# Kernel tuning notes

Hardware: AMD Instinct MI355X
Metric: run time of the kernel (lower is better)

## Reference

```python
import jax, jax.numpy as jnp
import numpy as np

S, D, H = 1024, 512, 4
DK = D // H  # 128
POOL = 16
EPS = 1e-5


def _pos_encoding(seq_len, dmodel):
    pos = jnp.arange(seq_len, dtype=jnp.float32)[:, None]
    div = jnp.exp(jnp.arange(0, dmodel, 2, dtype=jnp.float32) * (-jnp.log(10000.0) / dmodel))
    ang = pos * div  # [S, D/2]
    # interleave sin/cos -> pe[:,0::2]=sin, pe[:,1::2]=cos
    return jnp.stack([jnp.sin(ang), jnp.cos(ang)], axis=-1).reshape(seq_len, dmodel)


def _layernorm(x, g, b):
    mu = jnp.mean(x, axis=-1, keepdims=True)
    var = jnp.var(x, axis=-1, keepdims=True)
    return (x - mu) * jax.lax.rsqrt(var + EPS) * g + b


def setup_inputs() -> dict:
    key = jax.random.key(0)
    ks = jax.random.split(key, 16)
    u = lambda k, shape, r: jax.random.uniform(k, shape, jnp.float32, -r, r)
    nfeature = 512
    return {
        "x": jax.random.normal(ks[0], (16, S, nfeature), jnp.float32),
        "emb_w": u(ks[1], (nfeature, D), (1.0 / nfeature) ** 0.5),
        "emb_b": u(ks[2], (D,), (1.0 / nfeature) ** 0.5),
        "WQ": u(ks[3], (H, D, DK), 0.1),
        "WK": u(ks[4], (H, D, DK), 0.1),
        "WV": u(ks[5], (H, D, DK), 0.1),
        "WO": u(ks[6], (H * DK, D), 0.1),
        "g1": jnp.ones((D,), jnp.float32),
        "b1": jnp.zeros((D,), jnp.float32),
        "l1_w": u(ks[7], (D, 4 * D), (1.0 / D) ** 0.5),
        "l1_b": u(ks[8], (4 * D,), (1.0 / D) ** 0.5),
        "l2_w": u(ks[9], (4 * D, D), (1.0 / (4 * D)) ** 0.5),
        "l2_b": u(ks[10], (D,), (1.0 / (4 * D)) ** 0.5),
        "g2": jnp.ones((D,), jnp.float32),
        "b2": jnp.zeros((D,), jnp.float32),
        "fc_w": u(ks[11], (S * (D // POOL), 2), 0.1),
        "fc_b": jnp.zeros((2,), jnp.float32),
    }


def reference(x, emb_w, emb_b, WQ, WK, WV, WO, g1, b1, l1_w, l1_b, l2_w, l2_b, g2, b2, fc_w, fc_b):
    # dropout layers are identity (eval mode)
    h = x @ emb_w + emb_b                       # [B,S,D]
    h = h.reshape(-1, S, D) + _pos_encoding(S, D)
    inp = h
    # per-head projections (hand-rolled MHA)
    Qi = jnp.einsum('bsd,hde->bhse', h, WQ)     # [B,H,S,DK]
    Ki = jnp.einsum('bsd,hde->bhse', h, WK)
    Vi = jnp.einsum('bsd,hde->bhse', h, WV)
    scores = jnp.einsum('bhse,bhte->bhst', Qi, Ki) / jnp.sqrt(jnp.float32(DK))
    attn = jax.nn.softmax(scores, axis=-1)      # [B,H,S,S] -- full attention matrix, as in source
    head = jnp.einsum('bhst,bhte->bhse', attn, Vi)  # [B,H,S,DK]
    # NOTE: source does a raw reshape [B,H,S,DK] -> [B,S,H*DK] (no transpose); replicate exactly
    out = head.reshape(-1, S, H * DK) @ WO      # [B,S,D]
    h = _layernorm(out + inp, g1, b1)
    ffn = jax.nn.relu(h @ l1_w + l1_b) @ l2_w + l2_b
    h = _layernorm(ffn + h, g2, b2)
    # MaxPool1d(16,16) over the feature dim: [B,S,512] -> [B,S,32]
    pooled = h.reshape(-1, S, D // POOL, POOL).max(axis=-1)
    logits = pooled.reshape(-1, S * (D // POOL)) @ fc_w + fc_b  # [B,2]
    return jax.nn.log_softmax(logits, axis=-1)
```

## Files before the change

### kernel.cpp

```cpp
#include <hip/hip_runtime.h>

typedef unsigned short ushortb;
typedef __attribute__((ext_vector_type(8))) short short8;
typedef __attribute__((ext_vector_type(4))) float f32x4;

__device__ __forceinline__ ushortb f2bb(float f) {
    union { float f; unsigned u; } x; x.f = f;
    unsigned r = x.u + 0x7fffu + ((x.u >> 16) & 1u);
    return (ushortb)(r >> 16);
}
__device__ __forceinline__ float bb2f(ushortb u) {
    union { unsigned u; float f; } x; x.u = ((unsigned)u) << 16; return x.f;
}

__device__ __forceinline__ unsigned pkbb(float a, float b) {
#if __has_builtin(__builtin_amdgcn_cvt_pk_bf16_f32)
    auto p = __builtin_amdgcn_cvt_pk_bf16_f32(a, b);
    unsigned u; __builtin_memcpy(&u, &p, 4);
    return u;
#else
    return (unsigned)f2bb(a) | ((unsigned)f2bb(b) << 16);
#endif
}

#if __has_builtin(__builtin_amdgcn_exp2f)
#define EXP2(x) __builtin_amdgcn_exp2f(x)
#else
#define EXP2(x) exp2f(x)
#endif

__device__ __forceinline__ void async_ld16(void* lds, const void* g) {
    __builtin_amdgcn_global_load_lds(
        (const __attribute__((address_space(1))) void*)g,
        (__attribute__((address_space(3))) void*)lds, 16, 0, 0);
}

#define EP_EMB       0
#define EP_RES       2
#define EP_BIAS_RELU 3
#define EP_BIAS_RES  4
#define EP_QKV       7

template <int EP>
__global__ __launch_bounds__(256) void gemm_mfma(
    const ushortb* __restrict__ A, const ushortb* __restrict__ Bt,
    const float* __restrict__ bias, const ushortb* __restrict__ res,
    const float* __restrict__ pe, ushortb* __restrict__ C,
    int M, int N, int K)
{
    __shared__ ushortb sA[2][128][64];
    __shared__ ushortb sB[2][128][64];

    const int tid = threadIdx.x;
    const int wave = tid >> 6, lane = tid & 63;
    const int quad = lane >> 4, l15 = lane & 15;
    const int row0 = blockIdx.x * 128;
    const int col0 = blockIdx.y * 128;
    const int wm = (wave >> 1) * 64, wn = (wave & 1) * 64;
    const int srl = lane >> 3, slot = lane & 7;

    f32x4 acc[4][4];
    #pragma unroll
    for (int i = 0; i < 4; ++i)
        #pragma unroll
        for (int j = 0; j < 4; ++j) acc[i][j] = (f32x4){0.f, 0.f, 0.f, 0.f};

    #pragma unroll
    for (int c = 0; c < 4; ++c) {
        int rbase = wave * 32 + c * 8;
        int r = rbase + srl;
        int ka = (slot ^ ((r ^ (r >> 3)) & 7)) * 8;
        async_ld16(&sA[0][rbase][0], A  + (size_t)(row0 + r) * K + ka);
        async_ld16(&sB[0][rbase][0], Bt + (size_t)(col0 + r) * K + ka);
    }

    int buf = 0;
    for (int k0 = 0; k0 < K; k0 += 64) {
        __syncthreads();
        if (k0 + 64 < K) {
            int nb = buf ^ 1;
            #pragma unroll
            for (int c = 0; c < 4; ++c) {
                int rbase = wave * 32 + c * 8;
                int r = rbase + srl;
                int ka = (slot ^ ((r ^ (r >> 3)) & 7)) * 8;
                async_ld16(&sA[nb][rbase][0], A  + (size_t)(row0 + r) * K + k0 + 64 + ka);
                async_ld16(&sB[nb][rbase][0], Bt + (size_t)(col0 + r) * K + k0 + 64 + ka);
            }
        }
        #pragma unroll
        for (int kc = 0; kc < 2; ++kc) {
            short8 af[4], bf[4];
            #pragma unroll
            for (int i = 0; i < 4; ++i) {
                int m = wm + i * 16 + l15;
                af[i] = *(const short8*)&sA[buf][m][(((kc * 4 + quad) ^ ((m ^ (m >> 3)) & 7))) * 8];
            }
            #pragma unroll
            for (int j = 0; j < 4; ++j) {
                int n = wn + j * 16 + l15;
                bf[j] = *(const short8*)&sB[buf][n][(((kc * 4 + quad) ^ ((n ^ (n >> 3)) & 7))) * 8];
            }
            #pragma unroll
            for (int i = 0; i < 4; ++i)
                #pragma unroll
                for (int j = 0; j < 4; ++j)
                    acc[i][j] = __builtin_amdgcn_mfma_f32_16x16x32_bf16(af[i], bf[j], acc[i][j], 0, 0, 0);
        }
        buf ^= 1;
    }

    if constexpr (EP == EP_QKV) {
        if (col0 < 1024) {
            ushortb* dst = C + ((size_t)(col0 >> 9)) * ((size_t)M * 512);
            #pragma unroll
            for (int i = 0; i < 4; ++i)
                #pragma unroll
                for (int r = 0; r < 4; ++r) {
                    int row = row0 + wm + i * 16 + quad * 4 + r;
                    #pragma unroll
                    for (int j = 0; j < 4; ++j) {
                        int col = (col0 + wn + j * 16 + l15) & 511;
                        dst[(size_t)row * 512 + col] = f2bb(acc[i][j][r]);
                    }
                }
        } else {
            ushortb* Vt = C + (size_t)2 * M * 512;
            int bb_ = row0 >> 10;
            #pragma unroll
            for (int i = 0; i < 4; ++i) {
                int s = (row0 & 1023) + wm + i * 16 + quad * 4;
                #pragma unroll
                for (int j = 0; j < 4; ++j) {
                    int vcol = col0 + wn + j * 16 + l15 - 1024;
                    int h = vcol >> 7, e = vcol & 127;
                    uint2 v;
                    v.x = pkbb(acc[i][j][0], acc[i][j][1]);
                    v.y = pkbb(acc[i][j][2], acc[i][j][3]);
                    *(uint2*)&Vt[((size_t)((bb_ * 4 + h) * 128 + e) << 10) + s] = v;
                }
            }
        }
        return;
    }

    #pragma unroll
    for (int i = 0; i < 4; ++i) {
        #pragma unroll
        for (int r = 0; r < 4; ++r) {
            int row = row0 + wm + i * 16 + quad * 4 + r;
            #pragma unroll
            for (int j = 0; j < 4; ++j) {
                int col = col0 + wn + j * 16 + l15;
                float v = acc[i][j][r];
                if constexpr (EP == EP_EMB) {
                    v += bias[col] + pe[((row & 1023) << 9) + col];
                } else if constexpr (EP == EP_RES) {
                    v += bb2f(res[(size_t)row * N + col]);
                } else if constexpr (EP == EP_BIAS_RELU) {
                    v = fmaxf(v + bias[col], 0.0f);
                } else if constexpr (EP == EP_BIAS_RES) {
                    v += bias[col] + bb2f(res[(size_t)row * N + col]);
                }
                C[(size_t)row * N + col] = f2bb(v);
            }
        }
    }
}

__global__ __launch_bounds__(256) void conv_x(const float* __restrict__ in,
                                              ushortb* __restrict__ out)
{
    size_t i4 = (size_t)blockIdx.x * 256 + threadIdx.x;
    float4 v = *(const float4*)(in + i4 * 4);
    ushort4 o;
    o.x = f2bb(v.x); o.y = f2bb(v.y); o.z = f2bb(v.z); o.w = f2bb(v.w);
    *(ushort4*)(out + i4 * 4) = o;
}

__global__ __launch_bounds__(256) void tileT(const float* __restrict__ in,
                                             ushortb* __restrict__ out,
                                             int R, int C, float scale)
{
    __shared__ float t[64][65];
    const int tx = threadIdx.x & 63, ty = threadIdx.x >> 6;
    const int c0 = blockIdx.x * 64, r0 = blockIdx.y * 64;
    const size_t zoff = (size_t)blockIdx.z * R * C;
    #pragma unroll
    for (int i = 0; i < 16; ++i) {
        int r = ty + i * 4;
        t[r][tx] = in[zoff + (size_t)(r0 + r) * C + c0 + tx] * scale;
    }
    __syncthreads();
    #pragma unroll
    for (int i = 0; i < 16; ++i) {
        int r = ty + i * 4;
        out[zoff + (size_t)(c0 + r) * R + r0 + tx] = f2bb(t[tx][r]);
    }
}

__global__ __launch_bounds__(256) void pairT512(const float* __restrict__ emb_w,
                                                const float* __restrict__ WO,
                                                ushortb* __restrict__ embwt,
                                                ushortb* __restrict__ wot)
{
    __shared__ float t[64][65];
    const int tx = threadIdx.x & 63, ty = threadIdx.x >> 6;
    const int c0 = blockIdx.x * 64, r0 = blockIdx.y * 64;
    const float* in = blockIdx.z ? WO : emb_w;
    ushortb* out = blockIdx.z ? wot : embwt;
    #pragma unroll
    for (int i = 0; i < 16; ++i) {
        int r = ty + i * 4;
        t[r][tx] = in[(size_t)(r0 + r) * 512 + c0 + tx];
    }
    __syncthreads();
    #pragma unroll
    for (int i = 0; i < 16; ++i) {
        int r = ty + i * 4;
        out[(size_t)(c0 + r) * 512 + r0 + tx] = f2bb(t[tx][r]);
    }
}

__global__ __launch_bounds__(256) void qkvT(const float* __restrict__ WQ,
                                            const float* __restrict__ WK,
                                            const float* __restrict__ WV,
                                            ushortb* __restrict__ wqkvt,
                                            float qscale)
{
    __shared__ float t[64][65];
    const int tx = threadIdx.x & 63, ty = threadIdx.x >> 6;
    const int c0 = blockIdx.x * 64, r0 = blockIdx.y * 64;
    const int z = blockIdx.z, sel = z >> 2, zz = z & 3;
    const float* in = (sel == 0 ? WQ : (sel == 1 ? WK : WV)) + (size_t)zz * 65536;
    ushortb* out = wqkvt + (size_t)sel * 262144 + (size_t)zz * 65536;
    const float scale = (sel == 0) ? qscale : 1.0f;
    #pragma unroll
    for (int i = 0; i < 16; ++i) {
        int r = ty + i * 4;
        t[r][tx] = in[(size_t)(r0 + r) * 128 + c0 + tx] * scale;
    }
    __syncthreads();
    #pragma unroll
    for (int i = 0; i < 16; ++i) {
        int r = ty + i * 4;
        out[(size_t)(c0 + r) * 512 + r0 + tx] = f2bb(t[tx][r]);
    }
}

__global__ __launch_bounds__(256) void pe_kernel(float* __restrict__ pe)
{
    int idx = blockIdx.x * 256 + threadIdx.x;
    int s = idx >> 9, c = idx & 511;
    float div = expf((float)(c & ~1) * (-9.210340371976184f / 512.0f));
    float ang = (float)s * div;
    pe[idx] = (c & 1) ? cosf(ang) : sinf(ang);
}

__global__ __launch_bounds__(256) void attn_mfma(
    const ushortb* __restrict__ Qb, const ushortb* __restrict__ Kb,
    const ushortb* __restrict__ Vt, ushortb* __restrict__ O)
{
    __shared__ ushortb sK[2][32][128];
    __shared__ ushortb sVt[2][128][32];
    __shared__ ushortb sP[4][32][40];

    const int tid = threadIdx.x;
    const int wave = tid >> 6, lane = tid & 63;
    const int quad = lane >> 4, l15 = lane & 15;
    const int bid = blockIdx.x;
    const int bh = bid & 63, qc = bid >> 6;
    const int b = bh >> 2, h = bh & 3;
    const int q0 = qc * 128 + wave * 32;
    const size_t qk_off = ((size_t)b << 10) * 512 + h * 128;
    const ushortb* Qp = Qb + qk_off;
    const ushortb* Kp = Kb + qk_off;
    const ushortb* Vp = Vt + (((size_t)(b * 4 + h)) << 17);

    short8 qfA[4], qfB[4];
    {
        const ushortb* qa = Qp + (size_t)(q0 + l15) * 512;
        const ushortb* qb = Qp + (size_t)(q0 + 16 + l15) * 512;
        #pragma unroll
        for (int kc = 0; kc < 4; ++kc) {
            qfA[kc] = *(const short8*)(qa + kc * 32 + quad * 8);
            qfB[kc] = *(const short8*)(qb + kc * 32 + quad * 8);
        }
    }

    f32x4 oA[8], oB[8];
    #pragma unroll
    for (int dt = 0; dt < 8; ++dt) {
        oA[dt] = (f32x4){0.f, 0.f, 0.f, 0.f};
        oB[dt] = (f32x4){0.f, 0.f, 0.f, 0.f};
    }
    float lA = 0.f, lB = 0.f;

    #pragma unroll
    for (int c = 0; c < 2; ++c) {
        int seg = wave * 2 + c;
        int rk = seg * 4 + (lane >> 4);
        int ck = (lane & 15) ^ (rk & 15);
        async_ld16(&sK[0][seg * 4][0], Kp + (size_t)rk * 512 + ck * 8);
        int dv = seg * 16 + (lane >> 2);
        int cv = (lane & 3) ^ (dv & 3);
        async_ld16(&sVt[0][seg * 16][0], Vp + ((size_t)dv << 10) + cv * 8);
    }

    int buf = 0;
    for (int t0 = 0; t0 < 1024; t0 += 32) {
        __syncthreads();
        if (t0 + 32 < 1024) {
            int nb = buf ^ 1;
            #pragma unroll
            for (int c = 0; c < 2; ++c) {
                int seg = wave * 2 + c;
                int rk = seg * 4 + (lane >> 4);
                int ck = (lane & 15) ^ (rk & 15);
                async_ld16(&sK[nb][seg * 4][0], Kp + (size_t)(t0 + 32 + rk) * 512 + ck * 8);
                int dv = seg * 16 + (lane >> 2);
                int cv = (lane & 3) ^ (dv & 3);
                async_ld16(&sVt[nb][seg * 16][0], Vp + ((size_t)dv << 10) + t0 + 32 + cv * 8);
            }
        }

        f32x4 sA0 = {0,0,0,0}, sA1 = {0,0,0,0}, sB0 = {0,0,0,0}, sB1 = {0,0,0,0};
        #pragma unroll
        for (int kc = 0; kc < 4; ++kc) {
            short8 k0f = *(const short8*)&sK[buf][l15][((kc * 4 + quad) ^ l15) * 8];
            short8 k1f = *(const short8*)&sK[buf][16 + l15][((kc * 4 + quad) ^ l15) * 8];
            sA0 = __builtin_amdgcn_mfma_f32_16x16x32_bf16(k0f, qfA[kc], sA0, 0, 0, 0);
            sA1 = __builtin_amdgcn_mfma_f32_16x16x32_bf16(k1f, qfA[kc], sA1, 0, 0, 0);
            sB0 = __builtin_amdgcn_mfma_f32_16x16x32_bf16(k0f, qfB[kc], sB0, 0, 0, 0);
            sB1 = __builtin_amdgcn_mfma_f32_16x16x32_bf16(k1f, qfB[kc], sB1, 0, 0, 0);
        }

        float pA0[4], pA1[4], pB0[4], pB1[4];
        float sumA = 0.f, sumB = 0.f;
        #pragma unroll
        for (int r = 0; r < 4; ++r) {
            pA0[r] = EXP2(sA0[r]); pA1[r] = EXP2(sA1[r]);
            pB0[r] = EXP2(sB0[r]); pB1[r] = EXP2(sB1[r]);
            sumA += pA0[r] + pA1[r];
            sumB += pB0[r] + pB1[r];
        }
        lA += sumA; lB += sumB;

        uint2 w;
        w.x = pkbb(pA0[0], pA0[1]); w.y = pkbb(pA0[2], pA0[3]);
        *(uint2*)&sP[wave][l15][quad * 4] = w;
        w.x = pkbb(pA1[0], pA1[1]); w.y = pkbb(pA1[2], pA1[3]);
        *(uint2*)&sP[wave][l15][16 + quad * 4] = w;
        w.x = pkbb(pB0[0], pB0[1]); w.y = pkbb(pB0[2], pB0[3]);
        *(uint2*)&sP[wave][16 + l15][quad * 4] = w;
        w.x = pkbb(pB1[0], pB1[1]); w.y = pkbb(pB1[2], pB1[3]);
        *(uint2*)&sP[wave][16 + l15][16 + quad * 4] = w;

        short8 pfA = *(const short8*)&sP[wave][l15][quad * 8];
        short8 pfB = *(const short8*)&sP[wave][16 + l15][quad * 8];

        #pragma unroll
        for (int dt = 0; dt < 8; ++dt) {
            int d = dt * 16 + l15;
            short8 vfrag = *(const short8*)&sVt[buf][d][(quad ^ (d & 3)) * 8];
            oA[dt] = __builtin_amdgcn_mfma_f32_16x16x32_bf16(pfA, vfrag, oA[dt], 0, 0, 0);
            oB[dt] = __builtin_amdgcn_mfma_f32_16x16x32_bf16(pfB, vfrag, oB[dt], 0, 0, 0);
        }
        buf ^= 1;
    }

    lA += __shfl_xor(lA, 16); lA += __shfl_xor(lA, 32);
    lB += __shfl_xor(lB, 16); lB += __shfl_xor(lB, 32);

    const size_t obase = (((size_t)(b * 4 + h) << 10) + q0) << 7;
    #pragma unroll
    for (int r = 0; r < 4; ++r) {
        float invA = 1.0f / __shfl(lA, quad * 4 + r);
        float invB = 1.0f / __shfl(lB, quad * 4 + r);
        int qa = quad * 4 + r, qb = 16 + quad * 4 + r;
        #pragma unroll
        for (int dt = 0; dt < 8; ++dt) {
            O[obase + ((size_t)qa << 7) + dt * 16 + l15] = f2bb(oA[dt][r] * invA);
            O[obase + ((size_t)qb << 7) + dt * 16 + l15] = f2bb(oB[dt][r] * invB);
        }
    }
}

__global__ __launch_bounds__(256) void ln_kernel(const ushortb* __restrict__ in,
                                                 const float* __restrict__ g,
                                                 const float* __restrict__ bta,
                                                 ushortb* __restrict__ out)
{
    const int lane = threadIdx.x & 63, w = threadIdx.x >> 6;
    const size_t row = (size_t)blockIdx.x * 4 + w;
    const int e0 = lane * 8;
    short8 v8 = *(const short8*)(in + row * 512 + e0);
    float v[8];
    #pragma unroll
    for (int k = 0; k < 8; ++k) v[k] = bb2f((ushortb)((short*)&v8)[k]);
    float s = 0.f, sq = 0.f;
    #pragma unroll
    for (int k = 0; k < 8; ++k) { s += v[k]; sq += v[k] * v[k]; }
    #pragma unroll
    for (int o = 1; o < 64; o <<= 1) { s += __shfl_xor(s, o); sq += __shfl_xor(sq, o); }
    float mu = s * (1.0f / 512.0f);
    float var = sq * (1.0f / 512.0f) - mu * mu;
    float rstd = rsqrtf(var + 1e-5f);
    float4 g0 = *(const float4*)(g + e0),  g1 = *(const float4*)(g + e0 + 4);
    float4 b0 = *(const float4*)(bta + e0), b1 = *(const float4*)(bta + e0 + 4);
    float gg[8] = {g0.x, g0.y, g0.z, g0.w, g1.x, g1.y, g1.z, g1.w};
    float bb[8] = {b0.x, b0.y, b0.z, b0.w, b1.x, b1.y, b1.z, b1.w};
    short8 o8;
    #pragma unroll
    for (int k = 0; k < 8; ++k)
        ((short*)&o8)[k] = (short)f2bb((v[k] - mu) * rstd * gg[k] + bb[k]);
    *(short8*)(out + row * 512 + e0) = o8;
}

__global__ __launch_bounds__(256) void final_partial(const ushortb* __restrict__ ln2,
                                                     const float* __restrict__ fcw,
                                                     float* __restrict__ zbuf)
{
    const int b = blockIdx.x, chunk = blockIdx.y;
    const int tid = threadIdx.x;
    float a0 = 0.0f, a1 = 0.0f;
    #pragma unroll
    for (int t = 0; t < 8; ++t) {
        int m = chunk * 2048 + t * 256 + tid;
        int s = m >> 5, j = m & 31;
        const ushortb* p = ln2 + (((size_t)(b * 1024 + s)) << 9) + j * 16;
        float mx = -1e30f;
        #pragma unroll
        for (int e = 0; e < 16; ++e) mx = fmaxf(mx, bb2f(p[e]));
        a0 += mx * fcw[2 * m];
        a1 += mx * fcw[2 * m + 1];
    }
    __shared__ float r0[256], r1[256];
    r0[tid] = a0; r1[tid] = a1;
    __syncthreads();
    for (int o = 128; o > 0; o >>= 1) {
        if (tid < o) { r0[tid] += r0[tid + o]; r1[tid] += r1[tid + o]; }
        __syncthreads();
    }
    if (tid == 0) {
        atomicAdd(&zbuf[2 * b],     r0[0]);
        atomicAdd(&zbuf[2 * b + 1], r1[0]);
    }
}

__global__ __launch_bounds__(64) void final_logits(const float* __restrict__ zbuf,
                                                   const float* __restrict__ fcb,
                                                   float* __restrict__ out)
{
    int b = threadIdx.x;
    if (b < 16) {
        float z0 = zbuf[2 * b]     + fcb[0];
        float z1 = zbuf[2 * b + 1] + fcb[1];
        float mx = fmaxf(z0, z1);
        float lse = mx + logf(expf(z0 - mx) + expf(z1 - mx));
        out[2 * b]     = z0 - lse;
        out[2 * b + 1] = z1 - lse;
    }
}

extern "C" void kernel_launch(void* const* d_in, const int* in_sizes, int n_in,
                              void* d_out, int out_size, void* d_ws, size_t ws_size,
                              hipStream_t stream)
{
    const float* x     = (const float*)d_in[0];
    const float* emb_w = (const float*)d_in[1];
    const float* emb_b = (const float*)d_in[2];
    const float* WQ    = (const float*)d_in[3];
    const float* WK    = (const float*)d_in[4];
    const float* WV    = (const float*)d_in[5];
    const float* WO    = (const float*)d_in[6];
    const float* g1    = (const float*)d_in[7];
    const float* b1    = (const float*)d_in[8];
    const float* l1w   = (const float*)d_in[9];
    const float* l1b   = (const float*)d_in[10];
    const float* l2w   = (const float*)d_in[11];
    const float* l2b   = (const float*)d_in[12];
    const float* g2    = (const float*)d_in[13];
    const float* b2    = (const float*)d_in[14];
    const float* fcw   = (const float*)d_in[15];
    const float* fcb   = (const float*)d_in[16];
    float* out = (float*)d_out;

    char* ws = (char*)d_ws;
    const size_t Ub = (size_t)16384 * 512 * 2;
    ushortb* xb    = (ushortb*)(ws + 0 * Ub);
    ushortb* h0b   = (ushortb*)(ws + 1 * Ub);
    ushortb* Qb    = (ushortb*)(ws + 2 * Ub);
    ushortb* Kb    = (ushortb*)(ws + 3 * Ub);
    ushortb* Vt    = (ushortb*)(ws + 4 * Ub);
    ushortb* headR = (ushortb*)(ws + 5 * Ub);
    ushortb* mid   = (ushortb*)(ws + 3 * Ub);
    ushortb* r1    = xb;
    ushortb* ln1   = Qb;
    ushortb* r2    = xb;
    ushortb* ln2   = h0b;
    char* wb = ws + 7 * Ub;
    ushortb* embwt = (ushortb*)(wb);
    ushortb* wqkvt = (ushortb*)(wb + 524288);
    ushortb* wot   = (ushortb*)(wb + 2097152);
    ushortb* l1wt  = (ushortb*)(wb + 2621440);
    ushortb* l2wt  = (ushortb*)(wb + 4718592);
    float*   pe    = (float*)  (wb + 6815744);
    float*   zbuf  = (float*)  (wb + 8912896);

    const int M = 16384;
    const float qscale = 0.12753139626997592f;

    conv_x<<<8192, 256, 0, stream>>>(x, xb);
    pe_kernel<<<2048, 256, 0, stream>>>(pe);
    pairT512<<<dim3(8, 8, 2), 256, 0, stream>>>(emb_w, WO, embwt, wot);
    qkvT<<<dim3(2, 8, 12), 256, 0, stream>>>(WQ, WK, WV, wqkvt, qscale);
    tileT<<<dim3(32, 8, 1), 256, 0, stream>>>(l1w, l1wt, 512, 2048, 1.0f);
    tileT<<<dim3(8, 32, 1), 256, 0, stream>>>(l2w, l2wt, 2048, 512, 1.0f);
    hipMemsetAsync(zbuf, 0, 16 * 2 * sizeof(float), stream);

    gemm_mfma<EP_EMB><<<dim3(M / 128, 4), 256, 0, stream>>>(
        xb, embwt, emb_b, nullptr, pe, h0b, M, 512, 512);

    gemm_mfma<EP_QKV><<<dim3(M / 128, 12), 256, 0, stream>>>(
        h0b, wqkvt, nullptr, nullptr, nullptr, Qb, M, 1536, 512);

    attn_mfma<<<512, 256, 0, stream>>>(Qb, Kb, Vt, headR);

    gemm_mfma<EP_RES><<<dim3(M / 128, 4), 256, 0, stream>>>(
        headR, wot, nullptr, h0b, nullptr, r1, M, 512, 512);
    ln_kernel<<<M / 4, 256, 0, stream>>>(r1, g1, b1, ln1);

    gemm_mfma<EP_BIAS_RELU><<<dim3(M / 128, 16), 256, 0, stream>>>(
        ln1, l1wt, l1b, nullptr, nullptr, mid, M, 2048, 512);
    gemm_mfma<EP_BIAS_RES><<<dim3(M / 128, 4), 256, 0, stream>>>(
        mid, l2wt, l2b, ln1, nullptr, r2, M, 512, 2048);
    ln_kernel<<<M / 4, 256, 0, stream>>>(r2, g2, b2, ln2);

    final_partial<<<dim3(16, 16), 256, 0, stream>>>(ln2, fcw, zbuf);
    final_logits<<<1, 64, 0, stream>>>(zbuf, fcb, out);
}
```

Measured before the change: 356.4 us.

## Enlarge GEMM tiles to 128/256x256 with 8 waves and explicit waitcnt pipelining

```diff
diff --git a/kernel.cpp b/kernel.cpp
--- a/kernel.cpp
+++ b/kernel.cpp
@@ -41,80 +41,99 @@
 #define EP_BIAS_RES  4
 #define EP_QKV       7
 
-template <int EP>
-__global__ __launch_bounds__(256) void gemm_mfma(
+template <int EP, int BM>
+__global__ __launch_bounds__(512, 2) void gemm_big(
     const ushortb* __restrict__ A, const ushortb* __restrict__ Bt,
     const float* __restrict__ bias, const ushortb* __restrict__ res,
     const float* __restrict__ pe, ushortb* __restrict__ C,
     int M, int N, int K)
 {
-    __shared__ ushortb sA[2][128][64];
-    __shared__ ushortb sB[2][128][64];
+    constexpr int MI = BM / 32;
+    constexpr int CA = BM / 64;
+    __shared__ ushortb sA[2][BM][64];
+    __shared__ ushortb sB[2][256][64];
 
     const int tid = threadIdx.x;
     const int wave = tid >> 6, lane = tid & 63;
     const int quad = lane >> 4, l15 = lane & 15;
-    const int row0 = blockIdx.x * 128;
-    const int col0 = blockIdx.y * 128;
-    const int wm = (wave >> 1) * 64, wn = (wave & 1) * 64;
+    const int row0 = blockIdx.x * BM;
+    const int col0 = blockIdx.y * 256;
+    const int wm = (wave >> 2) * (BM / 2);
+    const int wn = (wave & 3) * 64;
     const int srl = lane >> 3, slot = lane & 7;
 
-    f32x4 acc[4][4];
-    #pragma unroll
-    for (int i = 0; i < 4; ++i)
+    f32x4 acc[MI][4];
+    #pragma unroll
+    for (int i = 0; i < MI; ++i)
         #pragma unroll
         for (int j = 0; j < 4; ++j) acc[i][j] = (f32x4){0.f, 0.f, 0.f, 0.f};
 
-    #pragma unroll
-    for (int c = 0; c < 4; ++c) {
-        int rbase = wave * 32 + c * 8;
-        int r = rbase + srl;
-        int ka = (slot ^ ((r ^ (r >> 3)) & 7)) * 8;
-        async_ld16(&sA[0][rbase][0], A  + (size_t)(row0 + r) * K + ka);
-        async_ld16(&sB[0][rbase][0], Bt + (size_t)(col0 + r) * K + ka);
-    }
-
-    int buf = 0;
-    for (int k0 = 0; k0 < K; k0 += 64) {
-        __syncthreads();
-        if (k0 + 64 < K) {
-            int nb = buf ^ 1;
-            #pragma unroll
-            for (int c = 0; c < 4; ++c) {
-                int rbase = wave * 32 + c * 8;
-                int r = rbase + srl;
-                int ka = (slot ^ ((r ^ (r >> 3)) & 7)) * 8;
-                async_ld16(&sA[nb][rbase][0], A  + (size_t)(row0 + r) * K + k0 + 64 + ka);
-                async_ld16(&sB[nb][rbase][0], Bt + (size_t)(col0 + r) * K + k0 + 64 + ka);
-            }
-        }
+    auto stage = [&](int b, int k0) {
+        #pragma unroll
+        for (int c = 0; c < CA; ++c) {
+            int rbase = (wave * CA + c) * 8;
+            int r = rbase + srl;
+            int ka = (slot ^ ((r ^ (r >> 3)) & 7)) * 8;
+            async_ld16(&sA[b][rbase][0], A + (size_t)(row0 + r) * K + k0 + ka);
+        }
+        #pragma unroll
+        for (int c = 0; c < 4; ++c) {
+            int rbase = (wave * 4 + c) * 8;
+            int r = rbase + srl;
+            int ka = (slot ^ ((r ^ (r >> 3)) & 7)) * 8;
+            async_ld16(&sB[b][rbase][0], Bt + (size_t)(col0 + r) * K + k0 + ka);
+        }
+    };
+
+    const int NT = K >> 6;
+    stage(0, 0);
+    stage(1, 64);
+    if constexpr (BM == 256) asm volatile("s_waitcnt vmcnt(8)" ::: "memory");
+    else                     asm volatile("s_waitcnt vmcnt(6)" ::: "memory");
+    __builtin_amdgcn_sched_barrier(0);
+    __builtin_amdgcn_s_barrier();
+
+    for (int t = 0; t < NT; ++t) {
+        const int b = t & 1;
         #pragma unroll
         for (int kc = 0; kc < 2; ++kc) {
-            short8 af[4], bf[4];
-            #pragma unroll
-            for (int i = 0; i < 4; ++i) {
+            short8 af[MI], bf[4];
+            #pragma unroll
+            for (int i = 0; i < MI; ++i) {
                 int m = wm + i * 16 + l15;
-                af[i] = *(const short8*)&sA[buf][m][(((kc * 4 + quad) ^ ((m ^ (m >> 3)) & 7))) * 8];
+                af[i] = *(const short8*)&sA[b][m][(((kc * 4 + quad) ^ ((m ^ (m >> 3)) & 7))) * 8];
             }
             #pragma unroll
             for (int j = 0; j < 4; ++j) {
                 int n = wn + j * 16 + l15;
-                bf[j] = *(const short8*)&sB[buf][n][(((kc * 4 + quad) ^ ((n ^ (n >> 3)) & 7))) * 8];
+                bf[j] = *(const short8*)&sB[b][n][(((kc * 4 + quad) ^ ((n ^ (n >> 3)) & 7))) * 8];
             }
             #pragma unroll
-            for (int i = 0; i < 4; ++i)
+            for (int i = 0; i < MI; ++i)
                 #pragma unroll
                 for (int j = 0; j < 4; ++j)
                     acc[i][j] = __builtin_amdgcn_mfma_f32_16x16x32_bf16(af[i], bf[j], acc[i][j], 0, 0, 0);
         }
-        buf ^= 1;
+        if (t == NT - 1) break;
+        asm volatile("s_waitcnt lgkmcnt(0)" ::: "memory");
+        __builtin_amdgcn_sched_barrier(0);
+        __builtin_amdgcn_s_barrier();
+        if (t + 2 < NT) {
+            stage(b, (t + 2) << 6);
+            if constexpr (BM == 256) asm volatile("s_waitcnt vmcnt(8)" ::: "memory");
+            else                     asm volatile("s_waitcnt vmcnt(6)" ::: "memory");
+        } else {
+            asm volatile("s_waitcnt vmcnt(0)" ::: "memory");
+        }
+        __builtin_amdgcn_sched_barrier(0);
+        __builtin_amdgcn_s_barrier();
     }
 
     if constexpr (EP == EP_QKV) {
         if (col0 < 1024) {
             ushortb* dst = C + ((size_t)(col0 >> 9)) * ((size_t)M * 512);
             #pragma unroll
-            for (int i = 0; i < 4; ++i)
+            for (int i = 0; i < MI; ++i)
                 #pragma unroll
                 for (int r = 0; r < 4; ++r) {
                     int row = row0 + wm + i * 16 + quad * 4 + r;
@@ -128,7 +147,7 @@
             ushortb* Vt = C + (size_t)2 * M * 512;
             int bb_ = row0 >> 10;
             #pragma unroll
-            for (int i = 0; i < 4; ++i) {
+            for (int i = 0; i < MI; ++i) {
                 int s = (row0 & 1023) + wm + i * 16 + quad * 4;
                 #pragma unroll
                 for (int j = 0; j < 4; ++j) {
@@ -145,7 +164,7 @@
     }
 
     #pragma unroll
-    for (int i = 0; i < 4; ++i) {
+    for (int i = 0; i < MI; ++i) {
         #pragma unroll
         for (int r = 0; r < 4; ++r) {
             int row = row0 + wm + i * 16 + quad * 4 + r;
@@ -519,21 +538,21 @@
     tileT<<<dim3(8, 32, 1), 256, 0, stream>>>(l2w, l2wt, 2048, 512, 1.0f);
     hipMemsetAsync(zbuf, 0, 16 * 2 * sizeof(float), stream);
 
-    gemm_mfma<EP_EMB><<<dim3(M / 128, 4), 256, 0, stream>>>(
+    gemm_big<EP_EMB, 128><<<dim3(M / 128, 2), 512, 0, stream>>>(
         xb, embwt, emb_b, nullptr, pe, h0b, M, 512, 512);
 
-    gemm_mfma<EP_QKV><<<dim3(M / 128, 12), 256, 0, stream>>>(
+    gemm_big<EP_QKV, 128><<<dim3(M / 128, 6), 512, 0, stream>>>(
         h0b, wqkvt, nullptr, nullptr, nullptr, Qb, M, 1536, 512);
 
     attn_mfma<<<512, 256, 0, stream>>>(Qb, Kb, Vt, headR);
 
-    gemm_mfma<EP_RES><<<dim3(M / 128, 4), 256, 0, stream>>>(
+    gemm_big<EP_RES, 128><<<dim3(M / 128, 2), 512, 0, stream>>>(
         headR, wot, nullptr, h0b, nullptr, r1, M, 512, 512);
     ln_kernel<<<M / 4, 256, 0, stream>>>(r1, g1, b1, ln1);
 
-    gemm_mfma<EP_BIAS_RELU><<<dim3(M / 128, 16), 256, 0, stream>>>(
+    gemm_big<EP_BIAS_RELU, 256><<<dim3(M / 256, 8), 512, 0, stream>>>(
         ln1, l1wt, l1b, nullptr, nullptr, mid, M, 2048, 512);
-    gemm_mfma<EP_BIAS_RES><<<dim3(M / 128, 4), 256, 0, stream>>>(
+    gemm_big<EP_BIAS_RES, 128><<<dim3(M / 128, 2), 512, 0, stream>>>(
         mid, l2wt, l2b, ln1, nullptr, r2, M, 512, 2048);
     ln_kernel<<<M / 4, 256, 0, stream>>>(r2, g2, b2, ln2);
 
```

New measurement: 367.5 us. +3.1%, slower.

## Deepen attention K/V prefetch to four LDS stages with explicit waitcnts

Applied to the files above, without the earlier changes.

```diff
diff --git a/kernel.cpp b/kernel.cpp
--- a/kernel.cpp
+++ b/kernel.cpp
@@ -28,6 +28,9 @@
 #else
 #define EXP2(x) exp2f(x)
 #endif
+
+#define WAITV(n) asm volatile("s_waitcnt vmcnt(" #n ")" ::: "memory")
+#define WAITL()  asm volatile("s_waitcnt lgkmcnt(0)" ::: "memory")
 
 __device__ __forceinline__ void async_ld16(void* lds, const void* g) {
     __builtin_amdgcn_global_load_lds(
@@ -261,8 +264,8 @@
     const ushortb* __restrict__ Qb, const ushortb* __restrict__ Kb,
     const ushortb* __restrict__ Vt, ushortb* __restrict__ O)
 {
-    __shared__ ushortb sK[2][32][128];
-    __shared__ ushortb sVt[2][128][32];
+    __shared__ ushortb sK[4][32][128];
+    __shared__ ushortb sVt[4][128][32];
     __shared__ ushortb sP[4][32][40];
 
     const int tid = threadIdx.x;
@@ -296,35 +299,34 @@
     }
     float lA = 0.f, lB = 0.f;
 
-    #pragma unroll
-    for (int c = 0; c < 2; ++c) {
-        int seg = wave * 2 + c;
-        int rk = seg * 4 + (lane >> 4);
-        int ck = (lane & 15) ^ (rk & 15);
-        async_ld16(&sK[0][seg * 4][0], Kp + (size_t)rk * 512 + ck * 8);
-        int dv = seg * 16 + (lane >> 2);
-        int cv = (lane & 3) ^ (dv & 3);
-        async_ld16(&sVt[0][seg * 16][0], Vp + ((size_t)dv << 10) + cv * 8);
-    }
-
-    int buf = 0;
-    for (int t0 = 0; t0 < 1024; t0 += 32) {
-        __syncthreads();
-        if (t0 + 32 < 1024) {
-            int nb = buf ^ 1;
-            #pragma unroll
-            for (int c = 0; c < 2; ++c) {
-                int seg = wave * 2 + c;
-                int rk = seg * 4 + (lane >> 4);
-                int ck = (lane & 15) ^ (rk & 15);
-                async_ld16(&sK[nb][seg * 4][0], Kp + (size_t)(t0 + 32 + rk) * 512 + ck * 8);
-                int dv = seg * 16 + (lane >> 2);
-                int cv = (lane & 3) ^ (dv & 3);
-                async_ld16(&sVt[nb][seg * 16][0], Vp + ((size_t)dv << 10) + t0 + 32 + cv * 8);
-            }
-        }
+    auto stage = [&](int bsel, int tt) {
+        #pragma unroll
+        for (int c = 0; c < 2; ++c) {
+            int seg = wave * 2 + c;
+            int rk = seg * 4 + (lane >> 4);
+            int ck = (lane & 15) ^ (rk & 15);
+            async_ld16(&sK[bsel][seg * 4][0], Kp + (size_t)(tt + rk) * 512 + ck * 8);
+            int dv = seg * 16 + (lane >> 2);
+            int cv = (lane & 3) ^ (dv & 3);
+            async_ld16(&sVt[bsel][seg * 16][0], Vp + ((size_t)dv << 10) + tt + cv * 8);
+        }
+    };
+
+    stage(0, 0);
+    stage(1, 32);
+    stage(2, 64);
+    WAITV(8);
+    __builtin_amdgcn_sched_barrier(0);
+    __builtin_amdgcn_s_barrier();
+    __builtin_amdgcn_sched_barrier(0);
+
+    #pragma unroll 4
+    for (int t = 0; t < 32; ++t) {
+        const int buf = t & 3;
+        if (t < 29) stage((t + 3) & 3, (t + 3) << 5);
 
         f32x4 sA0 = {0,0,0,0}, sA1 = {0,0,0,0}, sB0 = {0,0,0,0}, sB1 = {0,0,0,0};
+        __builtin_amdgcn_s_setprio(1);
         #pragma unroll
         for (int kc = 0; kc < 4; ++kc) {
             short8 k0f = *(const short8*)&sK[buf][l15][((kc * 4 + quad) ^ l15) * 8];
@@ -334,6 +336,7 @@
             sB0 = __builtin_amdgcn_mfma_f32_16x16x32_bf16(k0f, qfB[kc], sB0, 0, 0, 0);
             sB1 = __builtin_amdgcn_mfma_f32_16x16x32_bf16(k1f, qfB[kc], sB1, 0, 0, 0);
         }
+        __builtin_amdgcn_s_setprio(0);
 
         float pA0[4], pA1[4], pB0[4], pB1[4];
         float sumA = 0.f, sumB = 0.f;
@@ -359,6 +362,7 @@
         short8 pfA = *(const short8*)&sP[wave][l15][quad * 8];
         short8 pfB = *(const short8*)&sP[wave][16 + l15][quad * 8];
 
+        __builtin_amdgcn_s_setprio(1);
         #pragma unroll
         for (int dt = 0; dt < 8; ++dt) {
             int d = dt * 16 + l15;
@@ -366,7 +370,16 @@
             oA[dt] = __builtin_amdgcn_mfma_f32_16x16x32_bf16(pfA, vfrag, oA[dt], 0, 0, 0);
             oB[dt] = __builtin_amdgcn_mfma_f32_16x16x32_bf16(pfB, vfrag, oB[dt], 0, 0, 0);
         }
-        buf ^= 1;
+        __builtin_amdgcn_s_setprio(0);
+
+        if (t == 31) break;
+        WAITL();
+        if (t <= 28)      { WAITV(8); }
+        else if (t == 29) { WAITV(4); }
+        else              { WAITV(0); }
+        __builtin_amdgcn_sched_barrier(0);
+        __builtin_amdgcn_s_barrier();
+        __builtin_amdgcn_sched_barrier(0);
     }
 
     lA += __shfl_xor(lA, 16); lA += __shfl_xor(lA, 32);
```

After: 363.0 us. No clear change (+1.9%).

## Add 256x256 tiled GEMM for FFN up-projection and widen attention KV stages

Applied to the files above, without the earlier changes.

```diff
diff --git a/kernel.cpp b/kernel.cpp
--- a/kernel.cpp
+++ b/kernel.cpp
@@ -168,6 +168,89 @@
     }
 }
 
+__global__ __launch_bounds__(512, 2) void gemm_256(
+    const ushortb* __restrict__ A, const ushortb* __restrict__ Bt,
+    const float* __restrict__ bias, ushortb* __restrict__ C,
+    int M, int N, int K)
+{
+    __shared__ ushortb sA[2][256][64];
+    __shared__ ushortb sB[2][256][64];
+
+    const int tid = threadIdx.x;
+    const int wave = tid >> 6, lane = tid & 63;
+    const int quad = lane >> 4, l15 = lane & 15;
+    const int row0 = blockIdx.x * 256;
+    const int col0 = blockIdx.y * 256;
+    const int wm = (wave >> 2) * 128;
+    const int wn = (wave & 3) * 64;
+    const int srl = lane >> 3, slot = lane & 7;
+
+    f32x4 acc[8][4];
+    #pragma unroll
+    for (int i = 0; i < 8; ++i)
+        #pragma unroll
+        for (int j = 0; j < 4; ++j) acc[i][j] = (f32x4){0.f, 0.f, 0.f, 0.f};
+
+    #pragma unroll
+    for (int c = 0; c < 4; ++c) {
+        int rbase = wave * 32 + c * 8;
+        int r = rbase + srl;
+        int ka = (slot ^ ((r ^ (r >> 3)) & 7)) * 8;
+        async_ld16(&sA[0][rbase][0], A  + (size_t)(row0 + r) * K + ka);
+        async_ld16(&sB[0][rbase][0], Bt + (size_t)(col0 + r) * K + ka);
+    }
+
+    int buf = 0;
+    for (int k0 = 0; k0 < K; k0 += 64) {
+        __syncthreads();
+        if (k0 + 64 < K) {
+            int nb = buf ^ 1;
+            #pragma unroll
+            for (int c = 0; c < 4; ++c) {
+                int rbase = wave * 32 + c * 8;
+                int r = rbase + srl;
+                int ka = (slot ^ ((r ^ (r >> 3)) & 7)) * 8;
+                async_ld16(&sA[nb][rbase][0], A  + (size_t)(row0 + r) * K + k0 + 64 + ka);
+                async_ld16(&sB[nb][rbase][0], Bt + (size_t)(col0 + r) * K + k0 + 64 + ka);
+            }
+        }
+        #pragma unroll
+        for (int kc = 0; kc < 2; ++kc) {
+            short8 af[8], bf[4];
+            #pragma unroll
+            for (int i = 0; i < 8; ++i) {
+                int m = wm + i * 16 + l15;
+                af[i] = *(const short8*)&sA[buf][m][(((kc * 4 + quad) ^ ((m ^ (m >> 3)) & 7))) * 8];
+            }
+            #pragma unroll
+            for (int j = 0; j < 4; ++j) {
+                int n = wn + j * 16 + l15;
+                bf[j] = *(const short8*)&sB[buf][n][(((kc * 4 + quad) ^ ((n ^ (n >> 3)) & 7))) * 8];
+            }
+            #pragma unroll
+            for (int i = 0; i < 8; ++i)
+                #pragma unroll
+                for (int j = 0; j < 4; ++j)
+                    acc[i][j] = __builtin_amdgcn_mfma_f32_16x16x32_bf16(af[i], bf[j], acc[i][j], 0, 0, 0);
+        }
+        buf ^= 1;
+    }
+
+    #pragma unroll
+    for (int i = 0; i < 8; ++i) {
+        #pragma unroll
+        for (int r = 0; r < 4; ++r) {
+            int row = row0 + wm + i * 16 + quad * 4 + r;
+            #pragma unroll
+            for (int j = 0; j < 4; ++j) {
+                int col = col0 + wn + j * 16 + l15;
+                float v = fmaxf(acc[i][j][r] + bias[col], 0.0f);
+                C[(size_t)row * N + col] = f2bb(v);
+            }
+        }
+    }
+}
+
 __global__ __launch_bounds__(256) void conv_x(const float* __restrict__ in,
                                               ushortb* __restrict__ out)
 {
@@ -261,8 +344,8 @@
     const ushortb* __restrict__ Qb, const ushortb* __restrict__ Kb,
     const ushortb* __restrict__ Vt, ushortb* __restrict__ O)
 {
-    __shared__ ushortb sK[2][32][128];
-    __shared__ ushortb sVt[2][128][32];
+    __shared__ ushortb sK[2][2][32][128];
+    __shared__ ushortb sVt[2][2][128][32];
     __shared__ ushortb sP[4][32][40];
 
     const int tid = threadIdx.x;
@@ -297,74 +380,85 @@
     float lA = 0.f, lB = 0.f;
 
     #pragma unroll
-    for (int c = 0; c < 2; ++c) {
-        int seg = wave * 2 + c;
-        int rk = seg * 4 + (lane >> 4);
-        int ck = (lane & 15) ^ (rk & 15);
-        async_ld16(&sK[0][seg * 4][0], Kp + (size_t)rk * 512 + ck * 8);
-        int dv = seg * 16 + (lane >> 2);
-        int cv = (lane & 3) ^ (dv & 3);
-        async_ld16(&sVt[0][seg * 16][0], Vp + ((size_t)dv << 10) + cv * 8);
+    for (int s = 0; s < 2; ++s) {
+        #pragma unroll
+        for (int c = 0; c < 2; ++c) {
+            int seg = wave * 2 + c;
+            int rk = seg * 4 + (lane >> 4);
+            int ck = (lane & 15) ^ (rk & 15);
+            async_ld16(&sK[0][s][seg * 4][0], Kp + (size_t)(s * 32 + rk) * 512 + ck * 8);
+            int dv = seg * 16 + (lane >> 2);
+            int cv = (lane & 3) ^ (dv & 3);
+            async_ld16(&sVt[0][s][seg * 16][0], Vp + ((size_t)dv << 10) + s * 32 + cv * 8);
+        }
     }
 
     int buf = 0;
-    for (int t0 = 0; t0 < 1024; t0 += 32) {
+    for (int t0 = 0; t0 < 1024; t0 += 64) {
         __syncthreads();
-        if (t0 + 32 < 1024) {
+        if (t0 + 64 < 1024) {
             int nb = buf ^ 1;
             #pragma unroll
-            for (int c = 0; c < 2; ++c) {
-                int seg = wave * 2 + c;
-                int rk = seg * 4 + (lane >> 4);
-                int ck = (lane & 15) ^ (rk & 15);
-                async_ld16(&sK[nb][seg * 4][0], Kp + (size_t)(t0 + 32 + rk) * 512 + ck * 8);
-                int dv = seg * 16 + (lane >> 2);
-                int cv = (lane & 3) ^ (dv & 3);
-                async_ld16(&sVt[nb][seg * 16][0], Vp + ((size_t)dv << 10) + t0 + 32 + cv * 8);
-            }
-        }
-
-        f32x4 sA0 = {0,0,0,0}, sA1 = {0,0,0,0}, sB0 = {0,0,0,0}, sB1 = {0,0,0,0};
-        #pragma unroll
-        for (int kc = 0; kc < 4; ++kc) {
-            short8 k0f = *(const short8*)&sK[buf][l15][((kc * 4 + quad) ^ l15) * 8];
-            short8 k1f = *(const short8*)&sK[buf][16 + l15][((kc * 4 + quad) ^ l15) * 8];
-            sA0 = __builtin_amdgcn_mfma_f32_16x16x32_bf16(k0f, qfA[kc], sA0, 0, 0, 0);
-            sA1 = __builtin_amdgcn_mfma_f32_16x16x32_bf16(k1f, qfA[kc], sA1, 0, 0, 0);
-            sB0 = __builtin_amdgcn_mfma_f32_16x16x32_bf16(k0f, qfB[kc], sB0, 0, 0, 0);
-            sB1 = __builtin_amdgcn_mfma_f32_16x16x32_bf16(k1f, qfB[kc], sB1, 0, 0, 0);
-        }
-
-        float pA0[4], pA1[4], pB0[4], pB1[4];
-        float sumA = 0.f, sumB = 0.f;
-        #pragma unroll
-        for (int r = 0; r < 4; ++r) {
-            pA0[r] = EXP2(sA0[r]); pA1[r] = EXP2(sA1[r]);
-            pB0[r] = EXP2(sB0[r]); pB1[r] = EXP2(sB1[r]);
-            sumA += pA0[r] + pA1[r];
-            sumB += pB0[r] + pB1[r];
-        }
-        lA += sumA; lB += sumB;
-
-        uint2 w;
-        w.x = pkbb(pA0[0], pA0[1]); w.y = pkbb(pA0[2], pA0[3]);
-        *(uint2*)&sP[wave][l15][quad * 4] = w;
-        w.x = pkbb(pA1[0], pA1[1]); w.y = pkbb(pA1[2], pA1[3]);
-        *(uint2*)&sP[wave][l15][16 + quad * 4] = w;
-        w.x = pkbb(pB0[0], pB0[1]); w.y = pkbb(pB0[2], pB0[3]);
-        *(uint2*)&sP[wave][16 + l15][quad * 4] = w;
-        w.x = pkbb(pB1[0], pB1[1]); w.y = pkbb(pB1[2], pB1[3]);
-        *(uint2*)&sP[wave][16 + l15][16 + quad * 4] = w;
-
-        short8 pfA = *(const short8*)&sP[wave][l15][quad * 8];
-        short8 pfB = *(const short8*)&sP[wave][16 + l15][quad * 8];
-
-        #pragma unroll
-        for (int dt = 0; dt < 8; ++dt) {
-            int d = dt * 16 + l15;
-            short8 vfrag = *(const short8*)&sVt[buf][d][(quad ^ (d & 3)) * 8];
-            oA[dt] = __builtin_amdgcn_mfma_f32_16x16x32_bf16(pfA, vfrag, oA[dt], 0, 0, 0);
-            oB[dt] = __builtin_amdgcn_mfma_f32_16x16x32_bf16(pfB, vfrag, oB[dt], 0, 0, 0);
+            for (int s = 0; s < 2; ++s) {
+                #pragma unroll
+                for (int c = 0; c < 2; ++c) {
+                    int seg = wave * 2 + c;
+                    int rk = seg * 4 + (lane >> 4);
+                    int ck = (lane & 15) ^ (rk & 15);
+                    async_ld16(&sK[nb][s][seg * 4][0],
+                               Kp + (size_t)(t0 + 64 + s * 32 + rk) * 512 + ck * 8);
+                    int dv = seg * 16 + (lane >> 2);
+                    int cv = (lane & 3) ^ (dv & 3);
+                    async_ld16(&sVt[nb][s][seg * 16][0],
+                               Vp + ((size_t)dv << 10) + t0 + 64 + s * 32 + cv * 8);
+                }
+            }
+        }
+
+        #pragma unroll
+        for (int sub = 0; sub < 2; ++sub) {
+            f32x4 sA0 = {0,0,0,0}, sA1 = {0,0,0,0}, sB0 = {0,0,0,0}, sB1 = {0,0,0,0};
+            #pragma unroll
+            for (int kc = 0; kc < 4; ++kc) {
+                short8 k0f = *(const short8*)&sK[buf][sub][l15][((kc * 4 + quad) ^ l15) * 8];
+                short8 k1f = *(const short8*)&sK[buf][sub][16 + l15][((kc * 4 + quad) ^ l15) * 8];
+                sA0 = __builtin_amdgcn_mfma_f32_16x16x32_bf16(k0f, qfA[kc], sA0, 0, 0, 0);
+                sA1 = __builtin_amdgcn_mfma_f32_16x16x32_bf16(k1f, qfA[kc], sA1, 0, 0, 0);
+                sB0 = __builtin_amdgcn_mfma_f32_16x16x32_bf16(k0f, qfB[kc], sB0, 0, 0, 0);
+                sB1 = __builtin_amdgcn_mfma_f32_16x16x32_bf16(k1f, qfB[kc], sB1, 0, 0, 0);
+            }
+
+            float pA0[4], pA1[4], pB0[4], pB1[4];
+            float sumA = 0.f, sumB = 0.f;
+            #pragma unroll
+            for (int r = 0; r < 4; ++r) {
+                pA0[r] = EXP2(sA0[r]); pA1[r] = EXP2(sA1[r]);
+                pB0[r] = EXP2(sB0[r]); pB1[r] = EXP2(sB1[r]);
+                sumA += pA0[r] + pA1[r];
+                sumB += pB0[r] + pB1[r];
+            }
+            lA += sumA; lB += sumB;
+
+            uint2 w;
+            w.x = pkbb(pA0[0], pA0[1]); w.y = pkbb(pA0[2], pA0[3]);
+            *(uint2*)&sP[wave][l15][quad * 4] = w;
+            w.x = pkbb(pA1[0], pA1[1]); w.y = pkbb(pA1[2], pA1[3]);
+            *(uint2*)&sP[wave][l15][16 + quad * 4] = w;
+            w.x = pkbb(pB0[0], pB0[1]); w.y = pkbb(pB0[2], pB0[3]);
+            *(uint2*)&sP[wave][16 + l15][quad * 4] = w;
+            w.x = pkbb(pB1[0], pB1[1]); w.y = pkbb(pB1[2], pB1[3]);
+            *(uint2*)&sP[wave][16 + l15][16 + quad * 4] = w;
+
+            short8 pfA = *(const short8*)&sP[wave][l15][quad * 8];
+            short8 pfB = *(const short8*)&sP[wave][16 + l15][quad * 8];
+
+            #pragma unroll
+            for (int dt = 0; dt < 8; ++dt) {
+                int d = dt * 16 + l15;
+                short8 vfrag = *(const short8*)&sVt[buf][sub][d][(quad ^ (d & 3)) * 8];
+                oA[dt] = __builtin_amdgcn_mfma_f32_16x16x32_bf16(pfA, vfrag, oA[dt], 0, 0, 0);
+                oB[dt] = __builtin_amdgcn_mfma_f32_16x16x32_bf16(pfB, vfrag, oB[dt], 0, 0, 0);
+            }
         }
         buf ^= 1;
     }
@@ -531,8 +625,8 @@
         headR, wot, nullptr, h0b, nullptr, r1, M, 512, 512);
     ln_kernel<<<M / 4, 256, 0, stream>>>(r1, g1, b1, ln1);
 
-    gemm_mfma<EP_BIAS_RELU><<<dim3(M / 128, 16), 256, 0, stream>>>(
-        ln1, l1wt, l1b, nullptr, nullptr, mid, M, 2048, 512);
+    gemm_256<<<dim3(M / 256, 8), 512, 0, stream>>>(
+        ln1, l1wt, l1b, mid, M, 2048, 512);
     gemm_mfma<EP_BIAS_RES><<<dim3(M / 128, 4), 256, 0, stream>>>(
         mid, l2wt, l2b, ln1, nullptr, r2, M, 512, 2048);
     ln_kernel<<<M / 4, 256, 0, stream>>>(r2, g2, b2, ln2);
```

Measured after the change: 349.2 us. 2.0% less time.
